# Performance work log

Hardware: AMD Instinct MI355X
Metric: run time of the kernel (lower is better)

Reference implementation:

```python
import jax, jax.numpy as jnp
import numpy as np

N = 50000; E = 800000
IN = 128; OUT = 128; H = 2; C = OUT // H  # 64
MSG = 64; TDIM = 32; EDIM = MSG + TDIM  # 96


def setup_inputs() -> dict:
    key = jax.random.key(0)
    ks = jax.random.split(key, 16)
    x = jax.random.normal(ks[0], (N, IN), dtype=jnp.float32)
    last_update = jax.random.uniform(ks[1], (N,), dtype=jnp.float32)
    t = jax.random.uniform(ks[2], (E,), dtype=jnp.float32)
    msg = jax.random.normal(ks[3], (E, MSG), dtype=jnp.float32)
    edge_index = jax.random.randint(ks[4], (2, E), 0, N, dtype=jnp.int64)
    s = 1.0 / np.sqrt(IN)
    se = 1.0 / np.sqrt(EDIM)
    W_time = jax.random.normal(ks[5], (1, TDIM), dtype=jnp.float32)
    b_time = jnp.zeros((TDIM,), dtype=jnp.float32)
    W_q = jax.random.normal(ks[6], (IN, H * C), dtype=jnp.float32) * s
    b_q = jnp.zeros((H * C,), dtype=jnp.float32)
    W_k = jax.random.normal(ks[7], (IN, H * C), dtype=jnp.float32) * s
    b_k = jnp.zeros((H * C,), dtype=jnp.float32)
    W_v = jax.random.normal(ks[8], (IN, H * C), dtype=jnp.float32) * s
    b_v = jnp.zeros((H * C,), dtype=jnp.float32)
    W_e = jax.random.normal(ks[9], (EDIM, H * C), dtype=jnp.float32) * se
    b_e = jnp.zeros((H * C,), dtype=jnp.float32)
    W_skip = jax.random.normal(ks[10], (IN, H * C), dtype=jnp.float32) * s
    b_skip = jnp.zeros((H * C,), dtype=jnp.float32)
    return dict(x=x, last_update=last_update, t=t, msg=msg, edge_index=edge_index,
                W_time=W_time, b_time=b_time, W_q=W_q, b_q=b_q, W_k=W_k, b_k=b_k,
                W_v=W_v, b_v=b_v, W_e=W_e, b_e=b_e, W_skip=W_skip, b_skip=b_skip)


def reference(x, last_update, t, msg, edge_index,
              W_time, b_time, W_q, b_q, W_k, b_k, W_v, b_v,
              W_e, b_e, W_skip, b_skip):
    src = edge_index[0]  # message source (x_j)
    dst = edge_index[1]  # message target (x_i), softmax segments
    # TGN TimeEncoder: cos(Linear(1 -> TDIM))
    rel_t = last_update[src] - t                      # [E]
    rel_t_enc = jnp.cos(rel_t[:, None] * W_time[0][None, :] + b_time)  # [E, TDIM]
    edge_attr = jnp.concatenate([rel_t_enc, msg], axis=-1)             # [E, EDIM]
    # TransformerConv projections (eval mode: dropout off)
    q = (x @ W_q + b_q).reshape(N, H, C)
    k = (x @ W_k + b_k).reshape(N, H, C)
    v = (x @ W_v + b_v).reshape(N, H, C)
    e = (edge_attr @ W_e + b_e).reshape(E, H, C)
    k_j = k[src] + e                                   # [E, H, C]
    alpha = jnp.einsum('ehc,ehc->eh', q[dst], k_j) / jnp.sqrt(jnp.float32(C))
    # segment softmax over destination nodes (PyG softmax semantics)
    amax = jax.ops.segment_max(alpha, dst, num_segments=N)   # [N, H]
    ex = jnp.exp(alpha - amax[dst])                          # [E, H]
    denom = jax.ops.segment_sum(ex, dst, num_segments=N)     # [N, H]
    attn = ex / (denom[dst] + 1e-16)                         # [E, H]
    out = jax.ops.segment_sum(attn[:, :, None] * (v[src] + e), dst, num_segments=N)
    out = out.reshape(N, H * C)
    # root/skip connection (root_weight=True, beta=False)
    out = out + (x @ W_skip + b_skip)
    return out


if __name__ == '__main__':
    inp = setup_inputs()
    print(reference(**inp).shape)
```

## Files before the change

kernel.cpp:

```cpp
#include <hip/hip_runtime.h>

#define NN 50000
#define EE 800000
#define ATTN_BLOCKS 1024
#define ATTN_WAVES (ATTN_BLOCKS * 4)

using bf16x8 = __attribute__((ext_vector_type(8))) short;
using f32x4  = __attribute__((ext_vector_type(4))) float;
using u16x8  = __attribute__((ext_vector_type(8))) unsigned short;

__device__ __forceinline__ float b2f(unsigned short u) {
    return __uint_as_float(((unsigned)u) << 16);
}
__device__ __forceinline__ unsigned short f2b(float f) {
    unsigned u = __float_as_uint(f);
    u += 0x7FFF + ((u >> 16) & 1);
    return (unsigned short)(u >> 16);
}

__global__ void prep_kernel(const float* __restrict__ Wq,
                            const float* __restrict__ Wk,
                            const float* __restrict__ Wv,
                            const float* __restrict__ Ws,
                            const float* __restrict__ We,
                            unsigned short* __restrict__ Wt,
                            unsigned short* __restrict__ Wet,
                            int* __restrict__ deg) {
    int i = blockIdx.x * 256 + threadIdx.x;
    if (i < 512 * 128) {
        int n = i >> 7, k = i & 127;
        const float* W = (n < 128) ? Wq : (n < 256) ? Wk : (n < 384) ? Wv : Ws;
        Wt[i] = f2b(W[k * 128 + (n & 127)]);
    } else if (i < 512 * 128 + 128 * 96) {
        int j = i - 512 * 128;
        int n = j / 96, k = j - n * 96;
        Wet[j] = f2b(We[k * 128 + n]);
    }
    if (i < NN) deg[i] = 0;
}

__global__ __launch_bounds__(256) void node_gemm(
        const float* __restrict__ X, const unsigned short* __restrict__ Wt,
        const float* __restrict__ bq, const float* __restrict__ bk,
        const float* __restrict__ bv, const float* __restrict__ bs,
        unsigned short* __restrict__ Qb, unsigned short* __restrict__ Kb,
        unsigned short* __restrict__ Vb, unsigned short* __restrict__ Sb) {
    __shared__ unsigned short Al[64][136];
    __shared__ unsigned short Bl[64][136];
    const int tid = threadIdx.x;
    const int m0 = blockIdx.x * 64;
    const int row = tid >> 2, seg = tid & 3;
    {
        int gr = m0 + row;
        float xv[32];
#pragma unroll
        for (int i = 0; i < 32; i++) xv[i] = 0.f;
        if (gr < NN) {
            const float4* s = (const float4*)(X + (size_t)gr * 128 + seg * 32);
#pragma unroll
            for (int i = 0; i < 8; i++) *(float4*)&xv[i * 4] = s[i];
        }
#pragma unroll
        for (int c = 0; c < 4; c++) {
            u16x8 h;
#pragma unroll
            for (int j = 0; j < 8; j++) h[j] = f2b(xv[c * 8 + j]);
            *(u16x8*)&Al[row][seg * 32 + c * 8] = h;
        }
    }
    const int wave = tid >> 6, lane = tid & 63, quad = lane >> 4, l16 = lane & 15;
    for (int n0t = 0; n0t < 8; n0t++) {
        __syncthreads();
        {
            const uint4* sb = (const uint4*)(Wt + (size_t)(n0t * 64 + row) * 128 + seg * 32);
            uint4 b0 = sb[0], b1 = sb[1], b2 = sb[2], b3 = sb[3];
            uint4* db = (uint4*)&Bl[row][seg * 32];
            db[0] = b0; db[1] = b1; db[2] = b2; db[3] = b3;
        }
        __syncthreads();
        f32x4 acc[4] = {{0.f,0.f,0.f,0.f},{0.f,0.f,0.f,0.f},{0.f,0.f,0.f,0.f},{0.f,0.f,0.f,0.f}};
#pragma unroll
        for (int kk = 0; kk < 4; kk++) {
            bf16x8 af = *(const bf16x8*)&Al[wave * 16 + l16][kk * 32 + quad * 8];
#pragma unroll
            for (int nf = 0; nf < 4; nf++) {
                bf16x8 bg = *(const bf16x8*)&Bl[nf * 16 + l16][kk * 32 + quad * 8];
                acc[nf] = __builtin_amdgcn_mfma_f32_16x16x32_bf16(af, bg, acc[nf], 0, 0, 0);
            }
        }
        const int sel = n0t >> 1;
        const float* bias    = sel == 0 ? bq : sel == 1 ? bk : sel == 2 ? bv : bs;
        unsigned short* outp = sel == 0 ? Qb : sel == 1 ? Kb : sel == 2 ? Vb : Sb;
#pragma unroll
        for (int nf = 0; nf < 4; nf++) {
            int col = (n0t & 1) * 64 + nf * 16 + l16;
            float bvl = bias[col];
#pragma unroll
            for (int r = 0; r < 4; r++) {
                int orow = m0 + wave * 16 + quad * 4 + r;
                if (orow < NN) outp[(size_t)orow * 128 + col] = f2b(acc[nf][r] + bvl);
            }
        }
    }
}

__global__ void deg_kernel(const int* __restrict__ ei, int* __restrict__ deg) {
    int e = blockIdx.x * 256 + threadIdx.x;
    if (e < EE) atomicAdd(&deg[ei[EE + e]], 1);
}

#define SCAN_BLKS 196

__global__ __launch_bounds__(256) void scan1_kernel(const int* __restrict__ deg,
                                                    int* __restrict__ off,
                                                    int* __restrict__ bsum) {
    __shared__ int sm[256];
    int tid = threadIdx.x;
    int i = blockIdx.x * 256 + tid;
    int v = (i < NN) ? deg[i] : 0;
    sm[tid] = v;
    __syncthreads();
    for (int d = 1; d < 256; d <<= 1) {
        int t = (tid >= d) ? sm[tid - d] : 0;
        __syncthreads();
        sm[tid] += t;
        __syncthreads();
    }
    if (i < NN) off[i] = sm[tid] - v;
    if (tid == 255) bsum[blockIdx.x] = sm[255];
}

__global__ __launch_bounds__(256) void scan2_kernel(int* __restrict__ bsum,
                                                    int* __restrict__ bpre,
                                                    int* __restrict__ off) {
    __shared__ int sm[256];
    int tid = threadIdx.x;
    int v = (tid < SCAN_BLKS) ? bsum[tid] : 0;
    sm[tid] = v;
    __syncthreads();
    for (int d = 1; d < 256; d <<= 1) {
        int t = (tid >= d) ? sm[tid - d] : 0;
        __syncthreads();
        sm[tid] += t;
        __syncthreads();
    }
    if (tid < SCAN_BLKS) bpre[tid] = sm[tid] - v;
    if (tid == 255) off[NN] = sm[255];
}

__global__ __launch_bounds__(256) void scan3_kernel(int* __restrict__ off,
                                                    const int* __restrict__ bpre,
                                                    int* __restrict__ cur) {
    int i = blockIdx.x * 256 + threadIdx.x;
    if (i < NN) {
        int o = off[i] + bpre[blockIdx.x];
        off[i] = o;
        cur[i] = o;
    }
}

__global__ void scatter_kernel(const int* __restrict__ ei, int* __restrict__ cur,
                               int* __restrict__ elist) {
    int e = blockIdx.x * 256 + threadIdx.x;
    if (e < EE) {
        int d = ei[EE + e];
        int p = atomicAdd(&cur[d], 1);
        elist[p] = e;
    }
}

__global__ __launch_bounds__(256) void attn_kernel(
        const unsigned short* __restrict__ Qb, const unsigned short* __restrict__ Kb,
        const unsigned short* __restrict__ Vb, const unsigned short* __restrict__ Sb,
        const unsigned short* __restrict__ Wet, const float* __restrict__ be,
        const float* __restrict__ wt,  const float* __restrict__ bt,
        const float* __restrict__ lu,  const float* __restrict__ tt,
        const float* __restrict__ msg, const int* __restrict__ ei,
        const int* __restrict__ off, const int* __restrict__ elist,
        float* __restrict__ outp) {
    __shared__ unsigned short Wl[128][104];
    __shared__ unsigned short ea[4][16][104];
    __shared__ int esrc[4][16];
    const int tid = threadIdx.x;
    {
        int r = tid >> 1, half = tid & 1;
        const uint4* s = (const uint4*)(Wet + r * 96 + half * 48);
        uint4* d = (uint4*)&Wl[r][half * 48];
#pragma unroll
        for (int i = 0; i < 6; i++) d[i] = s[i];
    }
    __syncthreads();
    const int wave = tid >> 6, lane = tid & 63, quad = lane >> 4, l16 = lane & 15;
    const int er = lane >> 2, part = lane & 3;
    float q_be[8], wtv[8], btv[8];
#pragma unroll
    for (int nf = 0; nf < 8; nf++) q_be[nf] = be[l16 + nf * 16];
#pragma unroll
    for (int j = 0; j < 8; j++) { wtv[j] = wt[part * 8 + j]; btv[j] = bt[part * 8 + j]; }

    const int wid = blockIdx.x * 4 + wave;
    for (int node = wid; node < NN; node += ATTN_WAVES) {
        const int e0 = off[node];
        const int dg = off[node + 1] - e0;
        float qv[8];
#pragma unroll
        for (int nf = 0; nf < 8; nf++) qv[nf] = b2f(Qb[(size_t)node * 128 + l16 + nf * 16]);
        float accv[8] = {0.f,0.f,0.f,0.f,0.f,0.f,0.f,0.f};
        float l0 = 0.f, l1 = 0.f;

        for (int tb = 0; tb < dg; tb += 16) {
            int cnt = dg - tb; if (cnt > 16) cnt = 16;
            __asm__ volatile("s_waitcnt lgkmcnt(0)" ::: "memory");
            int eid = -1, sid = 0;
            if (er < cnt) { eid = elist[e0 + tb + er]; sid = ei[eid]; }
            if (part == 0) esrc[wave][er] = sid;
            float mv[16];
#pragma unroll
            for (int i = 0; i < 16; i++) mv[i] = 0.f;
            if (eid >= 0) {
                const float4* mp = (const float4*)(msg + (size_t)eid * 64 + part * 16);
#pragma unroll
                for (int i = 0; i < 4; i++) *(float4*)&mv[i * 4] = mp[i];
            }
#pragma unroll
            for (int c = 0; c < 2; c++) {
                u16x8 h;
#pragma unroll
                for (int j = 0; j < 8; j++) h[j] = f2b(mv[c * 8 + j]);
                *(u16x8*)&ea[wave][er][32 + part * 16 + c * 8] = h;
            }
            u16x8 tv = {0,0,0,0,0,0,0,0};
            if (eid >= 0) {
                float rel = lu[sid] - tt[eid];
#pragma unroll
                for (int j = 0; j < 8; j++) tv[j] = f2b(__cosf(rel * wtv[j] + btv[j]));
            }
            *(u16x8*)&ea[wave][er][part * 8] = tv;
            __asm__ volatile("s_waitcnt lgkmcnt(0)" ::: "memory");

            f32x4 acc8[8];
#pragma unroll
            for (int nf = 0; nf < 8; nf++) {
                float b = q_be[nf];
                acc8[nf] = (f32x4){b, b, b, b};
            }
#pragma unroll
            for (int kk = 0; kk < 3; kk++) {
                bf16x8 af = *(const bf16x8*)&ea[wave][l16][kk * 32 + quad * 8];
#pragma unroll
                for (int nf = 0; nf < 8; nf++) {
                    bf16x8 bg = *(const bf16x8*)&Wl[l16 + nf * 16][kk * 32 + quad * 8];
                    acc8[nf] = __builtin_amdgcn_mfma_f32_16x16x32_bf16(af, bg, acc8[nf], 0, 0, 0);
                }
            }
#pragma unroll
            for (int r = 0; r < 4; r++) {
                int slot = quad * 4 + r;
                int ssid = esrc[wave][slot];
                const unsigned short* kp = Kb + (size_t)ssid * 128;
                float p0 = 0.f, p1 = 0.f;
#pragma unroll
                for (int nf = 0; nf < 8; nf++) {
                    float kj = b2f(kp[l16 + nf * 16]) + acc8[nf][r];
                    if (nf < 4) p0 += qv[nf] * kj; else p1 += qv[nf] * kj;
                }
#pragma unroll
                for (int m = 1; m < 16; m <<= 1) {
                    p0 += __shfl_xor(p0, m, 64);
                    p1 += __shfl_xor(p1, m, 64);
                }
                bool valid = slot < cnt;
                float ex0 = valid ? __expf(p0 * 0.125f) : 0.f;
                float ex1 = valid ? __expf(p1 * 0.125f) : 0.f;
                l0 += ex0; l1 += ex1;
                const unsigned short* vp = Vb + (size_t)ssid * 128;
#pragma unroll
                for (int nf = 0; nf < 8; nf++) {
                    float vv = b2f(vp[l16 + nf * 16]) + acc8[nf][r];
                    accv[nf] += (nf < 4 ? ex0 : ex1) * vv;
                }
            }
        }
#pragma unroll
        for (int m = 16; m < 64; m <<= 1) {
            l0 += __shfl_xor(l0, m, 64);
            l1 += __shfl_xor(l1, m, 64);
#pragma unroll
            for (int nf = 0; nf < 8; nf++) accv[nf] += __shfl_xor(accv[nf], m, 64);
        }
        float inv0 = 1.f / (l0 + 1e-16f), inv1 = 1.f / (l1 + 1e-16f);
#pragma unroll
        for (int j = 0; j < 2; j++) {
            int nf = quad * 2 + j;
            int col = l16 + nf * 16;
            float o = accv[nf] * (nf < 4 ? inv0 : inv1) + b2f(Sb[(size_t)node * 128 + col]);
            outp[(size_t)node * 128 + col] = o;
        }
    }
}

extern "C" void kernel_launch(void* const* d_in, const int* in_sizes, int n_in,
                              void* d_out, int out_size, void* d_ws, size_t ws_size,
                              hipStream_t stream) {
    (void)in_sizes; (void)n_in; (void)out_size; (void)ws_size;
    const float* x   = (const float*)d_in[0];
    const float* lu  = (const float*)d_in[1];
    const float* tt  = (const float*)d_in[2];
    const float* msg = (const float*)d_in[3];
    const int*   ei  = (const int*)d_in[4];
    const float* wt  = (const float*)d_in[5];
    const float* btm = (const float*)d_in[6];
    const float* Wq  = (const float*)d_in[7];
    const float* bq  = (const float*)d_in[8];
    const float* Wk  = (const float*)d_in[9];
    const float* bk  = (const float*)d_in[10];
    const float* Wv  = (const float*)d_in[11];
    const float* bv  = (const float*)d_in[12];
    const float* We  = (const float*)d_in[13];
    const float* be  = (const float*)d_in[14];
    const float* Ws  = (const float*)d_in[15];
    const float* bs  = (const float*)d_in[16];

    char* p = (char*)d_ws;
    auto alloc = [&](size_t bytes) -> char* {
        char* r = p; p += (bytes + 255) & ~(size_t)255; return r;
    };
    unsigned short* Qb   = (unsigned short*)alloc((size_t)NN * 128 * 2);
    unsigned short* Kb   = (unsigned short*)alloc((size_t)NN * 128 * 2);
    unsigned short* Vb   = (unsigned short*)alloc((size_t)NN * 128 * 2);
    unsigned short* Sb   = (unsigned short*)alloc((size_t)NN * 128 * 2);
    unsigned short* Wt   = (unsigned short*)alloc(512 * 128 * 2);
    unsigned short* Wet  = (unsigned short*)alloc(128 * 96 * 2);
    int* deg   = (int*)alloc(NN * 4);
    int* cur   = (int*)alloc(NN * 4);
    int* off   = (int*)alloc((NN + 1) * 4);
    int* elist = (int*)alloc((size_t)EE * 4);
    int* bsum  = (int*)alloc(SCAN_BLKS * 4);
    int* bpre  = (int*)alloc(SCAN_BLKS * 4);

    hipLaunchKernelGGL(prep_kernel, dim3(304), dim3(256), 0, stream,
                       Wq, Wk, Wv, Ws, We, Wt, Wet, deg);
    hipLaunchKernelGGL(node_gemm, dim3(782), dim3(256), 0, stream,
                       x, Wt, bq, bk, bv, bs, Qb, Kb, Vb, Sb);
    hipLaunchKernelGGL(deg_kernel, dim3((EE + 255) / 256), dim3(256), 0, stream, ei, deg);
    hipLaunchKernelGGL(scan1_kernel, dim3(SCAN_BLKS), dim3(256), 0, stream, deg, off, bsum);
    hipLaunchKernelGGL(scan2_kernel, dim3(1), dim3(256), 0, stream, bsum, bpre, off);
    hipLaunchKernelGGL(scan3_kernel, dim3(SCAN_BLKS), dim3(256), 0, stream, off, bpre, cur);
    hipLaunchKernelGGL(scatter_kernel, dim3((EE + 255) / 256), dim3(256), 0, stream,
                       ei, cur, elist);
    hipLaunchKernelGGL(attn_kernel, dim3(ATTN_BLOCKS), dim3(256), 0, stream,
                       Qb, Kb, Vb, Sb, Wet, be, wt, btm, lu, tt, msg, ei, off, elist,
                       (float*)d_out);
}
```

Before: 631.5 us.

## Prefetch next edge batch and restructure attention layout with per-edge lanes

Rewrites the per-node attention loop so each lane owns one edge: K/V rows are loaded as vectorized 16-byte chunks per edge, and the MFMA edge projection is transposed through shared memory so dot products need only two cross-quad shuffles. The next batch's edge ids, source ids, last_update and t are software-prefetched during the current batch, and the next node's offsets are prefetched too. It also changes the grid to 768 blocks with a 3-blocks-per-CU launch bound and vectorizes the output store. This trades more register pressure and extra LDS round-trips for fewer scattered scalar gathers and less exposed latency.

```diff
diff --git a/kernel.cpp b/kernel.cpp
--- a/kernel.cpp
+++ b/kernel.cpp
@@ -2,7 +2,7 @@
 
 #define NN 50000
 #define EE 800000
-#define ATTN_BLOCKS 1024
+#define ATTN_BLOCKS 768
 #define ATTN_WAVES (ATTN_BLOCKS * 4)
 
 using bf16x8 = __attribute__((ext_vector_type(8))) short;
@@ -169,7 +169,7 @@
     }
 }
 
-__global__ __launch_bounds__(256) void attn_kernel(
+__global__ __launch_bounds__(256, 3) void attn_kernel(
         const unsigned short* __restrict__ Qb, const unsigned short* __restrict__ Kb,
         const unsigned short* __restrict__ Vb, const unsigned short* __restrict__ Sb,
         const unsigned short* __restrict__ Wet, const float* __restrict__ be,
@@ -179,8 +179,7 @@
         const int* __restrict__ off, const int* __restrict__ elist,
         float* __restrict__ outp) {
     __shared__ unsigned short Wl[128][104];
-    __shared__ unsigned short ea[4][16][104];
-    __shared__ int esrc[4][16];
+    __shared__ float scrf[4][16][68];
     const int tid = threadIdx.x;
     {
         int r = tid >> 1, half = tid & 1;
@@ -198,103 +197,195 @@
 #pragma unroll
     for (int j = 0; j < 8; j++) { wtv[j] = wt[part * 8 + j]; btv[j] = bt[part * 8 + j]; }
 
-    const int wid = blockIdx.x * 4 + wave;
-    for (int node = wid; node < NN; node += ATTN_WAVES) {
-        const int e0 = off[node];
-        const int dg = off[node + 1] - e0;
-        float qv[8];
-#pragma unroll
-        for (int nf = 0; nf < 8; nf++) qv[nf] = b2f(Qb[(size_t)node * 128 + l16 + nf * 16]);
-        float accv[8] = {0.f,0.f,0.f,0.f,0.f,0.f,0.f,0.f};
+    int node = blockIdx.x * 4 + wave;
+    int pf_e0 = 0, pf_dg = 0;
+    if (node < NN) { pf_e0 = off[node]; pf_dg = off[node + 1] - pf_e0; }
+    int c_eid = -1, c_sid = 0; float c_lu = 0.f, c_tt = 0.f;
+    {
+        int c0 = pf_dg < 16 ? pf_dg : 16;
+        if (er < c0) { c_eid = elist[pf_e0 + er]; c_sid = ei[c_eid];
+                       c_lu = lu[c_sid]; c_tt = tt[c_eid]; }
+    }
+    for (; node < NN; node += ATTN_WAVES) {
+        const int e0 = pf_e0, dg = pf_dg;
+        {
+            int nn = node + ATTN_WAVES;
+            if (nn < NN) { pf_e0 = off[nn]; pf_dg = off[nn + 1] - pf_e0; }
+            else { pf_e0 = 0; pf_dg = 0; }
+        }
+        u16x8 qf[4];
+#pragma unroll
+        for (int kk = 0; kk < 4; kk++)
+            qf[kk] = *(const u16x8*)(Qb + (size_t)node * 128 + kk * 32 + quad * 8);
+        float accA[4][8];
+#pragma unroll
+        for (int kk = 0; kk < 4; kk++)
+#pragma unroll
+            for (int j = 0; j < 8; j++) accA[kk][j] = 0.f;
         float l0 = 0.f, l1 = 0.f;
 
         for (int tb = 0; tb < dg; tb += 16) {
             int cnt = dg - tb; if (cnt > 16) cnt = 16;
             __asm__ volatile("s_waitcnt lgkmcnt(0)" ::: "memory");
-            int eid = -1, sid = 0;
-            if (er < cnt) { eid = elist[e0 + tb + er]; sid = ei[eid]; }
-            if (part == 0) esrc[wave][er] = sid;
+            int sidv = __shfl(c_sid, l16 << 2, 64);
+            u16x8 kf[4], vf[4];
+            {
+                const unsigned short* kp = Kb + (size_t)sidv * 128 + quad * 8;
+                const unsigned short* vp = Vb + (size_t)sidv * 128 + quad * 8;
+#pragma unroll
+                for (int kk = 0; kk < 4; kk++) {
+                    kf[kk] = *(const u16x8*)(kp + kk * 32);
+                    vf[kk] = *(const u16x8*)(vp + kk * 32);
+                }
+            }
+            unsigned short* earow = (unsigned short*)&scrf[wave][er][0];
             float mv[16];
 #pragma unroll
             for (int i = 0; i < 16; i++) mv[i] = 0.f;
-            if (eid >= 0) {
-                const float4* mp = (const float4*)(msg + (size_t)eid * 64 + part * 16);
+            if (c_eid >= 0) {
+                const float4* mp = (const float4*)(msg + (size_t)c_eid * 64 + part * 16);
 #pragma unroll
                 for (int i = 0; i < 4; i++) *(float4*)&mv[i * 4] = mp[i];
             }
+            bool more = (tb + 16 < dg);
+            int nbase = more ? (e0 + tb + 16) : pf_e0;
+            int ndg   = more ? (dg - tb - 16) : pf_dg;
+            int ncnt  = ndg < 16 ? ndg : 16;
+            int n_eid = -1, n_sid = 0; float n_lu = 0.f, n_tt = 0.f;
+            if (er < ncnt) n_eid = elist[nbase + er];
 #pragma unroll
             for (int c = 0; c < 2; c++) {
                 u16x8 h;
 #pragma unroll
                 for (int j = 0; j < 8; j++) h[j] = f2b(mv[c * 8 + j]);
-                *(u16x8*)&ea[wave][er][32 + part * 16 + c * 8] = h;
-            }
-            u16x8 tv = {0,0,0,0,0,0,0,0};
-            if (eid >= 0) {
-                float rel = lu[sid] - tt[eid];
+                *(u16x8*)&earow[32 + part * 16 + c * 8] = h;
+            }
+            u16x8 tv = {0, 0, 0, 0, 0, 0, 0, 0};
+            if (c_eid >= 0) {
+                float rel = c_lu - c_tt;
 #pragma unroll
                 for (int j = 0; j < 8; j++) tv[j] = f2b(__cosf(rel * wtv[j] + btv[j]));
             }
-            *(u16x8*)&ea[wave][er][part * 8] = tv;
+            *(u16x8*)&earow[part * 8] = tv;
+            if (er < ncnt) n_sid = ei[n_eid];
             __asm__ volatile("s_waitcnt lgkmcnt(0)" ::: "memory");
-
+            __builtin_amdgcn_sched_barrier(0);
             f32x4 acc8[8];
 #pragma unroll
             for (int nf = 0; nf < 8; nf++) {
                 float b = q_be[nf];
                 acc8[nf] = (f32x4){b, b, b, b};
             }
+            const unsigned short* ea16 = (const unsigned short*)&scrf[wave][l16][0];
 #pragma unroll
             for (int kk = 0; kk < 3; kk++) {
-                bf16x8 af = *(const bf16x8*)&ea[wave][l16][kk * 32 + quad * 8];
+                bf16x8 af = *(const bf16x8*)&ea16[kk * 32 + quad * 8];
 #pragma unroll
                 for (int nf = 0; nf < 8; nf++) {
                     bf16x8 bg = *(const bf16x8*)&Wl[l16 + nf * 16][kk * 32 + quad * 8];
                     acc8[nf] = __builtin_amdgcn_mfma_f32_16x16x32_bf16(af, bg, acc8[nf], 0, 0, 0);
                 }
             }
-#pragma unroll
-            for (int r = 0; r < 4; r++) {
-                int slot = quad * 4 + r;
-                int ssid = esrc[wave][slot];
-                const unsigned short* kp = Kb + (size_t)ssid * 128;
-                float p0 = 0.f, p1 = 0.f;
-#pragma unroll
-                for (int nf = 0; nf < 8; nf++) {
-                    float kj = b2f(kp[l16 + nf * 16]) + acc8[nf][r];
-                    if (nf < 4) p0 += qv[nf] * kj; else p1 += qv[nf] * kj;
-                }
-#pragma unroll
-                for (int m = 1; m < 16; m <<= 1) {
-                    p0 += __shfl_xor(p0, m, 64);
-                    p1 += __shfl_xor(p1, m, 64);
-                }
-                bool valid = slot < cnt;
-                float ex0 = valid ? __expf(p0 * 0.125f) : 0.f;
-                float ex1 = valid ? __expf(p1 * 0.125f) : 0.f;
-                l0 += ex0; l1 += ex1;
-                const unsigned short* vp = Vb + (size_t)ssid * 128;
-#pragma unroll
-                for (int nf = 0; nf < 8; nf++) {
-                    float vv = b2f(vp[l16 + nf * 16]) + acc8[nf][r];
-                    accv[nf] += (nf < 4 ? ex0 : ex1) * vv;
-                }
-            }
-        }
-#pragma unroll
-        for (int m = 16; m < 64; m <<= 1) {
+            if (er < ncnt) { n_lu = lu[n_sid]; n_tt = tt[n_eid]; }
+            float ex0, ex1;
+            __asm__ volatile("" ::: "memory");
+#pragma unroll
+            for (int nf = 0; nf < 4; nf++)
+#pragma unroll
+                for (int r = 0; r < 4; r++)
+                    scrf[wave][quad * 4 + r][l16 + nf * 16] = acc8[nf][r];
+            __asm__ volatile("s_waitcnt lgkmcnt(0)" ::: "memory");
+            __builtin_amdgcn_sched_barrier(0);
+            float ef0[16];
+#pragma unroll
+            for (int kk = 0; kk < 2; kk++) {
+                *(float4*)&ef0[kk * 8 + 0] = *(const float4*)&scrf[wave][l16][kk * 32 + quad * 8];
+                *(float4*)&ef0[kk * 8 + 4] = *(const float4*)&scrf[wave][l16][kk * 32 + quad * 8 + 4];
+            }
+            {
+                float p0 = 0.f;
+#pragma unroll
+                for (int kk = 0; kk < 2; kk++)
+#pragma unroll
+                    for (int j = 0; j < 8; j++)
+                        p0 += b2f(qf[kk][j]) * (b2f(kf[kk][j]) + ef0[kk * 8 + j]);
+                p0 += __shfl_xor(p0, 16, 64);
+                p0 += __shfl_xor(p0, 32, 64);
+                ex0 = (l16 < cnt) ? __expf(p0 * 0.125f) : 0.f;
+                l0 += ex0;
+#pragma unroll
+                for (int kk = 0; kk < 2; kk++)
+#pragma unroll
+                    for (int j = 0; j < 8; j++)
+                        accA[kk][j] += ex0 * (b2f(vf[kk][j]) + ef0[kk * 8 + j]);
+            }
+            __asm__ volatile("s_waitcnt lgkmcnt(0)" ::: "memory");
+#pragma unroll
+            for (int nf = 0; nf < 4; nf++)
+#pragma unroll
+                for (int r = 0; r < 4; r++)
+                    scrf[wave][quad * 4 + r][l16 + nf * 16] = acc8[4 + nf][r];
+            __asm__ volatile("s_waitcnt lgkmcnt(0)" ::: "memory");
+            __builtin_amdgcn_sched_barrier(0);
+            float ef1[16];
+#pragma unroll
+            for (int kk = 0; kk < 2; kk++) {
+                *(float4*)&ef1[kk * 8 + 0] = *(const float4*)&scrf[wave][l16][kk * 32 + quad * 8];
+                *(float4*)&ef1[kk * 8 + 4] = *(const float4*)&scrf[wave][l16][kk * 32 + quad * 8 + 4];
+            }
+            {
+                float p1 = 0.f;
+#pragma unroll
+                for (int kk = 0; kk < 2; kk++)
+#pragma unroll
+                    for (int j = 0; j < 8; j++)
+                        p1 += b2f(qf[2 + kk][j]) * (b2f(kf[2 + kk][j]) + ef1[kk * 8 + j]);
+                p1 += __shfl_xor(p1, 16, 64);
+                p1 += __shfl_xor(p1, 32, 64);
+                ex1 = (l16 < cnt) ? __expf(p1 * 0.125f) : 0.f;
+                l1 += ex1;
+#pragma unroll
+                for (int kk = 0; kk < 2; kk++)
+#pragma unroll
+                    for (int j = 0; j < 8; j++)
+                        accA[2 + kk][j] += ex1 * (b2f(vf[2 + kk][j]) + ef1[kk * 8 + j]);
+            }
+            c_eid = n_eid; c_sid = n_sid; c_lu = n_lu; c_tt = n_tt;
+        }
+        if (dg == 0) {
+            int c0 = pf_dg < 16 ? pf_dg : 16;
+            c_eid = -1; c_sid = 0; c_lu = 0.f; c_tt = 0.f;
+            if (er < c0) { c_eid = elist[pf_e0 + er]; c_sid = ei[c_eid];
+                           c_lu = lu[c_sid]; c_tt = tt[c_eid]; }
+        }
+#pragma unroll
+        for (int m = 1; m < 16; m <<= 1) {
             l0 += __shfl_xor(l0, m, 64);
             l1 += __shfl_xor(l1, m, 64);
 #pragma unroll
-            for (int nf = 0; nf < 8; nf++) accv[nf] += __shfl_xor(accv[nf], m, 64);
+            for (int kk = 0; kk < 4; kk++)
+#pragma unroll
+                for (int j = 0; j < 8; j++)
+                    accA[kk][j] += __shfl_xor(accA[kk][j], m, 64);
         }
         float inv0 = 1.f / (l0 + 1e-16f), inv1 = 1.f / (l1 + 1e-16f);
-#pragma unroll
-        for (int j = 0; j < 2; j++) {
-            int nf = quad * 2 + j;
-            int col = l16 + nf * 16;
-            float o = accv[nf] * (nf < 4 ? inv0 : inv1) + b2f(Sb[(size_t)node * 128 + col]);
-            outp[(size_t)node * 128 + col] = o;
+        if (l16 < 2) {
+#pragma unroll
+            for (int kk = 0; kk < 4; kk++) {
+                float inv = kk < 2 ? inv0 : inv1;
+                int col = kk * 32 + quad * 8 + l16 * 4;
+                float a0 = l16 ? accA[kk][4] : accA[kk][0];
+                float a1 = l16 ? accA[kk][5] : accA[kk][1];
+                float a2 = l16 ? accA[kk][6] : accA[kk][2];
+                float a3 = l16 ? accA[kk][7] : accA[kk][3];
+                ushort4 sk = *(const ushort4*)(Sb + (size_t)node * 128 + col);
+                float4 o;
+                o.x = a0 * inv + b2f(sk.x);
+                o.y = a1 * inv + b2f(sk.y);
+                o.z = a2 * inv + b2f(sk.z);
+                o.w = a3 * inv + b2f(sk.w);
+                *(float4*)(outp + (size_t)node * 128 + col) = o;
+            }
         }
     }
 }
```

Result: slower. 786.7 us (+24.6%).
